# Optimization experiments

Hardware: AMD Instinct MI355X
Metric: run time of the kernel (lower is better)

## Reference

```python
import jax, jax.numpy as jnp
import numpy as np

EPS = 1e-6

def _ln(x):
    m = jnp.mean(x, axis=-1, keepdims=True)
    v = jnp.mean((x - m) ** 2, axis=-1, keepdims=True)
    return (x - m) * jax.lax.rsqrt(v + EPS)

def _quant(x):
    # dynamic per-token symmetric int8 quant (fused_kernels.quant_sum semantics)
    s = jnp.maximum(jnp.max(jnp.abs(x), axis=-1, keepdims=True) / 127.0, 1e-8)
    q = jnp.clip(jnp.round(x / s), -127.0, 127.0)
    return q, s, jnp.sum(q, axis=-1, keepdims=True)

def _w8a8(x, qw, sw, zw, b):
    # W8A8OF16LinearDynamicInputScale: int8 GEMM + zero-point correction via row sum
    q, s, qsum = _quant(x)
    acc = q @ qw.astype(jnp.float32).T - qsum * zw.astype(jnp.float32)
    return acc * (s * sw) + b

def _self_attn(xm, Wqkv, bqkv, Wo, bo, H):
    Bt, S, C = xm.shape
    hd = C // H
    qkv = (xm @ Wqkv.T + bqkv).reshape(Bt, S, 3, H, hd)
    q, k, v = qkv[:, :, 0], qkv[:, :, 1], qkv[:, :, 2]
    attn = jnp.einsum('bqhd,bkhd->bhqk', q * (hd ** -0.5), k).astype(jnp.float32)
    attn = jax.nn.softmax(attn, axis=-1)
    out = jnp.einsum('bhqk,bkhd->bqhd', attn, v).reshape(Bt, S, C)
    return out @ Wo.T + bo

def _cross_attn(x, y, qw_q, sw_q, zw_q, b_q, Wkv, bkv, qw_cp, sw_cp, zw_cp, b_cp, H):
    B, N, C = x.shape
    hd = C // H
    q = _w8a8(x, qw_q, sw_q, zw_q, b_q).reshape(B * N, H, hd)
    kv = (y.reshape(-1, C) @ Wkv.T + bkv).reshape(-1, 2, H, hd)
    k, v = kv[:, 0], kv[:, 1]
    # mask=None path: q (1,B*N,H,hd) attends over all B*M keys (flattened)
    attn = jnp.einsum('qhd,khd->hqk', q * (hd ** -0.5), k).astype(jnp.float32)
    attn = jax.nn.softmax(attn, axis=-1)
    out = jnp.einsum('hqk,khd->qhd', attn, v).reshape(B, N, C)
    return _w8a8(out, qw_cp, sw_cp, zw_cp, b_cp)

def setup_inputs() -> dict:
    key = jax.random.key(0)
    ks = iter(jax.random.split(key, 32))
    B, T, S, C, H, M = 2, 8, 256, 1152, 16, 224
    Dh = int(C * 4.0)
    r = lambda shape, sc=1.0: jax.random.normal(next(ks), shape, dtype=jnp.float32) * sc
    qi = lambda shape: jax.random.randint(next(ks), shape, -127, 128, dtype=jnp.int8)
    zi = lambda shape: jax.random.randint(next(ks), shape, -8, 9, dtype=jnp.int32)
    su = lambda shape: jax.random.uniform(next(ks), shape, minval=0.005, maxval=0.02, dtype=jnp.float32)
    return dict(
        x=r((B, T * S, C)), y=r((B, M, C)), t=r((B, 6 * C)),
        sst=r((6, C), C ** -0.5),
        Wqkv=r((3 * C, C), 0.02), bqkv=r((3 * C,), 0.02),
        Wo=r((C, C), 0.02), bo=r((C,), 0.02),
        Wkv=r((2 * C, C), 0.02), bkv=r((2 * C,), 0.02),
        qw_q=qi((C, C)), sw_q=su((C,)), zw_q=zi((C,)), b_q=r((C,), 0.02),
        qw_cp=qi((C, C)), sw_cp=su((C,)), zw_cp=zi((C,)), b_cp=r((C,), 0.02),
        qw_f1=qi((Dh, C)), sw_f1=su((Dh,)), zw_f1=zi((Dh,)), b_f1=r((Dh,), 0.02),
        qw_f2=qi((C, Dh)), sw_f2=su((C,)), zw_f2=zi((C,)), b_f2=r((C,), 0.02),
        num_heads=H, T=T, S=S,
    )

def reference(x, y, t, sst, Wqkv, bqkv, Wo, bo, Wkv, bkv,
              qw_q, sw_q, zw_q, b_q, qw_cp, sw_cp, zw_cp, b_cp,
              qw_f1, sw_f1, zw_f1, b_f1, qw_f2, sw_f2, zw_f2, b_f2,
              num_heads, T, S):
    B, N, C = x.shape
    mod = sst[None] + t.reshape(B, 6, C)  # (B,6,C)
    shift_msa, scale_msa, gate_msa, shift_mlp, scale_mlp, gate_mlp = (
        mod[:, 0:1], mod[:, 1:2], mod[:, 2:3], mod[:, 3:4], mod[:, 4:5], mod[:, 5:6])
    # --- self-attention (spatial, temporal=False): B (T S) C -> (B T) S C ---
    x_m = _ln(x) * (1.0 + scale_msa) + shift_msa
    x_m = x_m.reshape(B * T, S, C)
    x_m = _self_attn(x_m, Wqkv, bqkv, Wo, bo, num_heads).reshape(B, N, C)
    x = x + gate_msa * x_m  # fused_kernels.gate_residual
    # --- int8 cross-attention ---
    x = x + _cross_attn(x, y, qw_q, sw_q, zw_q, b_q, Wkv, bkv, qw_cp, sw_cp, zw_cp, b_cp, num_heads)
    # --- int8 MLP with fused gelu_quant_sum (tanh-approx GELU) ---
    x_m = _ln(x) * (1.0 + scale_mlp) + shift_mlp
    h = _w8a8(x_m, qw_f1, sw_f1, zw_f1, b_f1)
    h = jax.nn.gelu(h, approximate=True)
    h = _w8a8(h, qw_f2, sw_f2, zw_f2, b_f2)
    x = x + gate_mlp * h
    return x
```

## Files before the change

### kernel.cpp

```cpp
#include <hip/hip_runtime.h>
#include <stdint.h>

typedef unsigned short u16;
typedef _Float16 f16;
typedef f16    f16v8  __attribute__((ext_vector_type(8)));
typedef u16    u16v8  __attribute__((ext_vector_type(8)));
typedef float  f32x4  __attribute__((ext_vector_type(4)));
typedef int    i32x4  __attribute__((ext_vector_type(4)));
typedef int    i32x16 __attribute__((ext_vector_type(16)));

#define MFMA_F16(a,b,c)   __builtin_amdgcn_mfma_f32_16x16x32_f16((a),(b),(c),0,0,0)
#define MFMA_I8_32(a,b,c) __builtin_amdgcn_mfma_i32_32x32x32_i8((a),(b),(c),0,0,0)

__device__ __forceinline__ float b2f(u16 u){ union{unsigned u;float f;}v; v.u=((unsigned)u)<<16; return v.f; }
__device__ __forceinline__ u16 f2b(float f){ union{float f;unsigned u;}v; v.f=f;
  return (u16)((v.u + 0x7fffu + ((v.u>>16)&1u))>>16); }
__device__ __forceinline__ u16 f2h(float f){ f16 h = (f16)f; return __builtin_bit_cast(u16, h); }
__device__ __forceinline__ float h2f(u16 u){ return (float)__builtin_bit_cast(f16, u); }
__device__ __forceinline__ f16v8 ldh8(const u16* p){ return __builtin_bit_cast(f16v8, *(const u16v8*)p); }
__device__ __forceinline__ void gl2lds16(const void* g, void* l){
  __builtin_amdgcn_global_load_lds(
    (const __attribute__((address_space(1))) unsigned int*)g,
    (__attribute__((address_space(3))) unsigned int*)l,
    16, 0, 0);
}
__device__ __forceinline__ float gelu_t(float x){
  float u2 = -1.5957691216057308f*(x + 0.044715f*x*x*x);
  return x * __builtin_amdgcn_rcpf(1.f + __expf(u2));
}

__global__ void mod_add_k(const float* __restrict__ sst, const float* __restrict__ t, float* __restrict__ mod){
  int i = blockIdx.x*256 + threadIdx.x;
  if (i < 2*6*1152) mod[i] = sst[i % 6912] + t[i];
}
__global__ void split2h_k(const float* __restrict__ src, u16* __restrict__ hi, u16* __restrict__ lo, int n){
  int i = blockIdx.x*256 + threadIdx.x;
  if (i >= n) return;
  float v = src[i];
  f16 h = (f16)v;
  hi[i] = __builtin_bit_cast(u16, h);
  lo[i] = f2h(v - (float)h);
}
__global__ void cross_prep_k(const int* __restrict__ qw_q, int8_t* __restrict__ w8q,
                             const int* __restrict__ qw_cp, int8_t* __restrict__ w8cp,
                             const float* __restrict__ Wkv, u16* __restrict__ wkvh, u16* __restrict__ wkvl,
                             const float* __restrict__ y, u16* __restrict__ yf){
  const int S1 = 1327104, S2 = 2654208, S3 = 5308416, S4 = 5824512;
  int i = blockIdx.x*256 + threadIdx.x;
  if (i < S1){ w8q[i] = (int8_t)qw_q[i]; }
  else if (i < S2){ int j = i - S1; w8cp[j] = (int8_t)qw_cp[j]; }
  else if (i < S3){ int j = i - S2; float v = Wkv[j]; f16 h = (f16)v;
    wkvh[j] = __builtin_bit_cast(u16, h); wkvl[j] = f2h(v - (float)h); }
  else if (i < S4){ int j = i - S3; yf[j] = f2h(y[j]); }
}
__global__ void mlp_prep_k(const int* __restrict__ qw_f1, int8_t* __restrict__ w8f1,
                           const int* __restrict__ qw_f2, int8_t* __restrict__ w8f2){
  const int S1 = 5308416, S2 = 10616832;
  int i = blockIdx.x*256 + threadIdx.x;
  if (i < S1){ w8f1[i] = (int8_t)qw_f1[i]; }
  else if (i < S2){ int j = i - S1; w8f2[j] = (int8_t)qw_f2[j]; }
}
__global__ void ln_mod_f16_k(const float* __restrict__ src, u16* __restrict__ xf,
                             const float* __restrict__ mod, int shift_row, int scale_row){
  const int row = blockIdx.x, tid = threadIdx.x;
  const int b = row >> 11;
  const float* ms = mod + ((size_t)b*6 + shift_row)*1152;
  const float* mc = mod + ((size_t)b*6 + scale_row)*1152;
  __shared__ float r1[256], r2[256];
  float s = 0.f, sq = 0.f, vals[5]; int cnt = 0;
  for (int c = tid; c < 1152; c += 256){
    float v = src[(size_t)row*1152+c];
    vals[cnt++] = v; s += v; sq += v*v;
  }
  r1[tid]=s; r2[tid]=sq; __syncthreads();
  for (int st=128; st>0; st>>=1){ if (tid<st){ r1[tid]+=r1[tid+st]; r2[tid]+=r2[tid+st]; } __syncthreads(); }
  float mean = r1[0]*(1.f/1152.f);
  float var  = r2[0]*(1.f/1152.f) - mean*mean;
  float rstd = rsqrtf(var + 1e-6f);
  cnt = 0;
  for (int c = tid; c < 1152; c += 256){
    float v = (vals[cnt++]-mean)*rstd*(1.f+mc[c]) + ms[c];
    xf[(size_t)row*1152+c] = f2h(v);
  }
}
__global__ void rgq_k(const float* __restrict__ x, const float* __restrict__ ao,
                      const float* __restrict__ mod, int gate_row, float* __restrict__ xw,
                      int8_t* __restrict__ q8, float* __restrict__ s_out, int* __restrict__ q_out){
  const int row = blockIdx.x, tid = threadIdx.x;
  const int b = row >> 11;
  const float* mg = mod + ((size_t)b*6 + gate_row)*1152;
  __shared__ float r1[256];
  __shared__ int ri[256];
  float mx = 0.f, vals[5]; int cnt = 0;
  for (int c = tid; c < 1152; c += 256){
    float v = x[(size_t)row*1152+c] + mg[c]*ao[(size_t)row*1152+c];
    xw[(size_t)row*1152+c] = v;
    vals[cnt++] = v; mx = fmaxf(mx, fabsf(v));
  }
  r1[tid]=mx; __syncthreads();
  for (int st=128; st>0; st>>=1){ if (tid<st) r1[tid]=fmaxf(r1[tid],r1[tid+st]); __syncthreads(); }
  const float s_ = fmaxf(r1[0]*(1.f/127.f), 1e-8f);
  const float inv = 1.f/s_;
  int acc = 0; cnt = 0;
  for (int c = tid; c < 1152; c += 256){
    float q = rintf(vals[cnt++]*inv);
    q = fminf(fmaxf(q, -127.f), 127.f);
    q8[(size_t)row*1152+c] = (int8_t)q;
    acc += (int)q;
  }
  ri[tid]=acc; __syncthreads();
  for (int st=128; st>0; st>>=1){ if (tid<st) ri[tid]+=ri[tid+st]; __syncthreads(); }
  if (tid==0){ s_out[row]=s_; q_out[row]=ri[0]; }
}
__global__ void rlq_k(float* __restrict__ xw, const float* __restrict__ add,
                      const float* __restrict__ mod, int shift_row, int scale_row,
                      int8_t* __restrict__ q8, float* __restrict__ s_out, int* __restrict__ q_out){
  const int row = blockIdx.x, tid = threadIdx.x;
  const int b = row >> 11;
  const float* ms = mod + ((size_t)b*6 + shift_row)*1152;
  const float* mc = mod + ((size_t)b*6 + scale_row)*1152;
  __shared__ float r1[256], r2[256];
  __shared__ int ri[256];
  float s = 0.f, sq = 0.f, vals[5]; int cnt = 0;
  for (int c = tid; c < 1152; c += 256){
    float v = xw[(size_t)row*1152+c] + add[(size_t)row*1152+c];
    xw[(size_t)row*1152+c] = v;
    vals[cnt++] = v; s += v; sq += v*v;
  }
  r1[tid]=s; r2[tid]=sq; __syncthreads();
  for (int st=128; st>0; st>>=1){ if (tid<st){ r1[tid]+=r1[tid+st]; r2[tid]+=r2[tid+st]; } __syncthreads(); }
  float mean = r1[0]*(1.f/1152.f);
  float var  = r2[0]*(1.f/1152.f) - mean*mean;
  float rstd = rsqrtf(var + 1e-6f);
  __syncthreads();
  float mx = 0.f; cnt = 0;
  for (int c = tid; c < 1152; c += 256){
    float v = (vals[cnt]-mean)*rstd*(1.f+mc[c]) + ms[c];
    vals[cnt++] = v; mx = fmaxf(mx, fabsf(v));
  }
  r1[tid]=mx; __syncthreads();
  for (int st=128; st>0; st>>=1){ if (tid<st) r1[tid]=fmaxf(r1[tid],r1[tid+st]); __syncthreads(); }
  const float s_ = fmaxf(r1[0]*(1.f/127.f), 1e-8f);
  const float inv = 1.f/s_;
  int acc = 0; cnt = 0;
  for (int c = tid; c < 1152; c += 256){
    float q = rintf(vals[cnt++]*inv);
    q = fminf(fmaxf(q, -127.f), 127.f);
    q8[(size_t)row*1152+c] = (int8_t)q;
    acc += (int)q;
  }
  ri[tid]=acc; __syncthreads();
  for (int st=128; st>0; st>>=1){ if (tid<st) ri[tid]+=ri[tid+st]; __syncthreads(); }
  if (tid==0){ s_out[row]=s_; q_out[row]=ri[0]; }
}
template<int SRC_F32>
__global__ void quant_rows_k(const void* __restrict__ src, int C_,
                             int8_t* __restrict__ q8, float* __restrict__ s_out, int* __restrict__ q_out){
  const int row = blockIdx.x, tid = threadIdx.x;
  __shared__ float red[256];
  __shared__ int redi[256];
  float vals[18];
  float mx = 0.f; int cnt = 0;
  for (int c = tid; c < C_; c += 256){
    float v = SRC_F32 ? ((const float*)src)[(size_t)row*C_+c] : b2f(((const u16*)src)[(size_t)row*C_+c]);
    vals[cnt++] = v;
    mx = fmaxf(mx, fabsf(v));
  }
  red[tid]=mx; __syncthreads();
  for (int st=128; st>0; st>>=1){ if (tid<st) red[tid]=fmaxf(red[tid],red[tid+st]); __syncthreads(); }
  const float s_ = fmaxf(red[0]*(1.f/127.f), 1e-8f);
  const float inv = 1.f/s_;
  int acc = 0; cnt = 0;
  for (int c = tid; c < C_; c += 256){
    float q = rintf(vals[cnt++]*inv);
    q = fminf(fmaxf(q, -127.f), 127.f);
    q8[(size_t)row*C_+c] = (int8_t)q;
    acc += (int)q;
  }
  redi[tid]=acc; __syncthreads();
  for (int st=128; st>0; st>>=1){ if (tid<st) redi[tid]+=redi[tid+st]; __syncthreads(); }
  if (tid==0){ s_out[row]=s_; q_out[row]=redi[0]; }
}

template<int MODE>
__global__ __launch_bounds__(256,4) void gemm_f16k(
    const u16* __restrict__ Af, int lda,
    const u16* __restrict__ Wh, const u16* __restrict__ Wl, int ldw,
    const float* __restrict__ bias, float* __restrict__ out, int ldo, int M, int K,
    u16* __restrict__ e1, u16* __restrict__ e2){
  __shared__ u16 sA[128*32];
  __shared__ u16 sWh[128*32];
  __shared__ u16 sWl[128*32];
  const int tid = threadIdx.x, lane = tid & 63;
  const int wv = tid >> 6, wx = wv & 1, wy = wv >> 1;
  const int quad = lane >> 4, l16 = lane & 15;
  const int m0 = blockIdx.y*128, n0 = blockIdx.x*128;
  f32x4 acc[4][4];
  #pragma unroll
  for (int i=0;i<4;i++)
    #pragma unroll
    for (int j=0;j<4;j++) acc[i][j] = (f32x4){0.f,0.f,0.f,0.f};
  for (int k0=0; k0<K; k0+=32){
    #pragma unroll
    for (int r=0;r<2;r++){
      int slotbase = r*256 + wv*64;
      int slot = slotbase + lane;
      int row = slot >> 2;
      int col8 = ((slot ^ (row>>1)) & 3) * 8;
      int gm = m0 + row; if (gm > M-1) gm = M-1;
      size_t aoff = (size_t)gm*lda + k0 + col8;
      size_t woff = (size_t)(n0+row)*ldw + k0 + col8;
      gl2lds16(Af + aoff, &sA[(size_t)slotbase*8]);
      gl2lds16(Wh + woff, &sWh[(size_t)slotbase*8]);
      gl2lds16(Wl + woff, &sWl[(size_t)slotbase*8]);
    }
    __syncthreads();
    const int cs = ((quad ^ ((l16>>1)&3)) * 8);
    f16v8 a[4], bh[4], bl[4];
    #pragma unroll
    for (int i=0;i<4;i++) a[i] = ldh8(&sA[(wy*64+i*16+l16)*32 + cs]);
    #pragma unroll
    for (int j=0;j<4;j++){
      bh[j] = ldh8(&sWh[(wx*64+j*16+l16)*32 + cs]);
      bl[j] = ldh8(&sWl[(wx*64+j*16+l16)*32 + cs]);
    }
    #pragma unroll
    for (int i=0;i<4;i++)
      #pragma unroll
      for (int j=0;j<4;j++){
        acc[i][j] = MFMA_F16(a[i], bh[j], acc[i][j]);
        acc[i][j] = MFMA_F16(a[i], bl[j], acc[i][j]);
      }
    __syncthreads();
  }
  #pragma unroll
  for (int j=0;j<4;j++){
    int col = n0 + wx*64 + j*16 + l16;
    float bc = bias ? bias[col] : 0.f;
    #pragma unroll
    for (int i=0;i<4;i++)
      #pragma unroll
      for (int r=0;r<4;r++){
        int row = m0 + wy*64 + i*16 + quad*4 + r;
        if (row >= M) continue;
        float v = acc[i][j][r] + bc;
        if (MODE == 0){
          out[(size_t)row*ldo + col] = v;
        } else if (MODE == 1){
          if (col < 2304){
            e1[(size_t)row*2304 + col] = f2h(v);
          } else {
            int vc = col - 2304;
            int hd_ = vc/72, d = vc - hd_*72;
            int z = row >> 8, s2 = row & 255;
            e2[((size_t)(z*16+hd_)*80 + d)*256 + s2] = f2h(v);
          }
        } else {
          if (col < 1152){
            e1[(size_t)row*1152 + col] = f2h(v);
          } else {
            int vc = col - 1152;
            int hd_ = vc/72, d = vc - hd_*72;
            e2[((size_t)hd_*80 + d)*448 + row] = f2h(v);
          }
        }
      }
  }
}

#define QKV_NT 36
__global__ __launch_bounds__(512,2) void gemm_qkv_8ph(
    const u16* __restrict__ Af,
    const u16* __restrict__ Wh_, const u16* __restrict__ Wl_,
    const float* __restrict__ bias,
    u16* __restrict__ qkf, u16* __restrict__ vtf){
  extern __shared__ u16 sm[];
  char* smb = (char*)sm;
  const int tid = threadIdx.x, lane = tid & 63, wv = tid >> 6;
  const int wr = wv >> 2, wc = wv & 3;
  const int quad = lane >> 4, l16 = lane & 15;
  const int c = blockIdx.x & 7, bi = blockIdx.x >> 3;
  const int m0 = (((c>>1)<<2) + (bi&3)) << 8;
  const int n0 = ((c&1)*7 + (bi>>2)) << 8;

  const u16* gA[2]; const u16* gH[2]; const u16* gL[2];
  int sbase[2];
  #pragma unroll
  for (int r=0;r<2;r++){
    int slot = r*512 + tid;
    int row = slot >> 2;
    int col8 = ((slot ^ (row>>1)) & 3) * 8;
    sbase[r] = (r*512 + wv*64) * 16;
    gA[r] = Af + (size_t)(m0+row)*1152 + col8;
    int gn = n0 + row; if (gn > 3455) gn = 3455;
    gH[r] = Wh_ + (size_t)gn*1152 + col8;
    gL[r] = Wl_ + (size_t)gn*1152 + col8;
  }

  #define STG_A(t2,b) { size_t ko=(size_t)(t2)*32; \
    gl2lds16(gA[0]+ko, smb + (b)*49152 + sbase[0]); \
    gl2lds16(gA[1]+ko, smb + (b)*49152 + sbase[1]); }
  #define STG_H(t2,b) { size_t ko=(size_t)(t2)*32; \
    gl2lds16(gH[0]+ko, smb + (b)*49152 + 16384 + sbase[0]); \
    gl2lds16(gH[1]+ko, smb + (b)*49152 + 16384 + sbase[1]); }
  #define STG_L(t2,b) { size_t ko=(size_t)(t2)*32; \
    gl2lds16(gL[0]+ko, smb + (b)*49152 + 32768 + sbase[0]); \
    gl2lds16(gL[1]+ko, smb + (b)*49152 + 32768 + sbase[1]); }

  STG_A(0,0); STG_H(0,0); STG_L(0,0);
  STG_A(1,1); STG_H(1,1); STG_L(1,1);

  const int cs = (quad ^ ((l16>>1)&3)) * 8;
  const int arow = wr*128 + l16;
  const int wrow = wc*64 + l16;

  f32x4 acc[8][4];
  #pragma unroll
  for (int i=0;i<8;i++)
    #pragma unroll
    for (int j=0;j<4;j++) acc[i][j] = (f32x4){0.f,0.f,0.f,0.f};

  f16v8 bh[4], bl[4];

  #define PHASE(p, STAGE_STMT) { \
    const u16* bA = sm + cur*24576; \
    f16v8 a0 = ldh8(bA + (arow + (2*(p))*16)*32 + cs); \
    f16v8 a1 = ldh8(bA + (arow + (2*(p)+1)*16)*32 + cs); \
    if ((p)==0){ \
      const u16* bH = bA + 8192; \
      const u16* bL = bA + 16384; \
      _Pragma("unroll") \
      for (int j=0;j<4;j++){ \
        bh[j] = ldh8(bH + (wrow + j*16)*32 + cs); \
        bl[j] = ldh8(bL + (wrow + j*16)*32 + cs); \
      } \
    } \
    STAGE_STMT; \
    __builtin_amdgcn_s_barrier(); \
    asm volatile("s_waitcnt lgkmcnt(0)" ::: "memory"); \
    __builtin_amdgcn_sched_barrier(0); \
    __builtin_amdgcn_s_setprio(1); \
    _Pragma("unroll") \
    for (int j=0;j<4;j++){ \
      acc[2*(p)][j]   = MFMA_F16(a0, bh[j], acc[2*(p)][j]); \
      acc[2*(p)][j]   = MFMA_F16(a0, bl[j], acc[2*(p)][j]); \
      acc[2*(p)+1][j] = MFMA_F16(a1, bh[j], acc[2*(p)+1][j]); \
      acc[2*(p)+1][j] = MFMA_F16(a1, bl[j], acc[2*(p)+1][j]); \
    } \
    __builtin_amdgcn_s_setprio(0); \
    __builtin_amdgcn_s_barrier(); \
  }

  int cur = 0;
  for (int t = 0; t < QKV_NT-1; ++t){
    const int nxt = (cur == 0) ? 2 : cur - 1;
    asm volatile("s_waitcnt vmcnt(6)" ::: "memory");
    __builtin_amdgcn_s_barrier();
    __builtin_amdgcn_sched_barrier(0);
    const bool pf = (t < QKV_NT-2);
    PHASE(0, if (pf) STG_A(t+2,nxt));
    PHASE(1, if (pf) STG_H(t+2,nxt));
    PHASE(2, if (pf) STG_L(t+2,nxt));
    PHASE(3, );
    cur = (cur == 2) ? 0 : cur + 1;
  }
  asm volatile("s_waitcnt vmcnt(0)" ::: "memory");
  __builtin_amdgcn_s_barrier();
  __builtin_amdgcn_sched_barrier(0);
  PHASE(0, );
  PHASE(1, );
  PHASE(2, );
  PHASE(3, );

  #pragma unroll
  for (int j=0;j<4;j++){
    const int col = n0 + wc*64 + j*16 + l16;
    if (col < 3456){
      const float bc = bias[col];
      if (col < 2304){
        #pragma unroll
        for (int i=0;i<8;i++){
          const size_t rb = (size_t)(m0 + wr*128 + i*16 + quad*4)*2304 + col;
          #pragma unroll
          for (int r=0;r<4;r++)
            qkf[rb + (size_t)r*2304] = f2h(acc[i][j][r] + bc);
        }
      } else {
        const int vc = col - 2304;
        const int hd_ = vc/72, d = vc - hd_*72;
        #pragma unroll
        for (int i=0;i<8;i++){
          #pragma unroll
          for (int r=0;r<4;r++){
            const int row = m0 + wr*128 + i*16 + quad*4 + r;
            const int z = row >> 8, s2 = row & 255;
            vtf[((size_t)(z*16+hd_)*80 + d)*256 + s2] = f2h(acc[i][j][r] + bc);
          }
        }
      }
    }
  }
  #undef PHASE
  #undef STG_A
  #undef STG_H
  #undef STG_L
}

__global__ __launch_bounds__(256,4) void gemm_i8(
    const int8_t* __restrict__ A, int lda, const int8_t* __restrict__ W, int ldw,
    const float* __restrict__ rs, const int* __restrict__ rq,
    const float* __restrict__ sw, const int* __restrict__ zw, const float* __restrict__ bias,
    void* __restrict__ out, int ldo, int M, int K, int do_gelu, int out_f32,
    const float* __restrict__ xwf, const float* __restrict__ modf, int do_final){
  __shared__ int8_t As[128*128];
  __shared__ int8_t Bs[128*128];
  const int tid = threadIdx.x, lane = tid & 63, wv = tid >> 6;
  const int wx = wv & 1, wy = wv >> 1;
  const int l32 = lane & 31, g = lane >> 5;
  int n_idx = blockIdx.x, m_idx = blockIdx.y;
  {
    int nwg = gridDim.x*gridDim.y;
    if ((nwg & 7) == 0){
      int l = blockIdx.y*gridDim.x + blockIdx.x;
      int qq = nwg >> 3;
      int gidx = (l & 7)*qq + (l >> 3);
      n_idx = gidx / (int)gridDim.y;
      m_idx = gidx - n_idx*(int)gridDim.y;
    }
  }
  const int m0 = m_idx*128, n0 = n_idx*128;
  const int srow = lane >> 3, schunk = lane & 7;
  const int scol = ((schunk ^ srow) & 7) * 16;
  i32x16 acc[2][2];
  #pragma unroll
  for (int i=0;i<2;i++)
    #pragma unroll
    for (int j=0;j<2;j++)
      #pragma unroll
      for (int r=0;r<16;r++) acc[i][j][r] = 0;
  for (int k0 = 0; k0 < K; k0 += 128){
    #pragma unroll
    for (int i=0;i<4;i++){
      int rr = (i*4 + wv)*8;
      int gm = m0 + rr + srow; if (gm > M-1) gm = M-1;
      gl2lds16(A + (size_t)gm*lda + k0 + scol, &As[rr*128]);
      int gn = n0 + rr + srow;
      gl2lds16(W + (size_t)gn*ldw + k0 + scol, &Bs[rr*128]);
    }
    __syncthreads();
    #pragma unroll
    for (int kq=0; kq<4; kq++){
      i32x4 af[2], bw[2];
      #pragma unroll
      for (int i=0;i<2;i++){
        int row = wy*64 + i*32 + l32;
        int cs = (((kq*2 + g) ^ (row & 7))) * 16;
        af[i] = *(const i32x4*)&As[row*128 + cs];
      }
      #pragma unroll
      for (int j=0;j<2;j++){
        int row = wx*64 + j*32 + l32;
        int cs = (((kq*2 + g) ^ (row & 7))) * 16;
        bw[j] = *(const i32x4*)&Bs[row*128 + cs];
      }
      #pragma unroll
      for (int i=0;i<2;i++)
        #pragma unroll
        for (int j=0;j<2;j++)
          acc[i][j] = MFMA_I8_32(af[i], bw[j], acc[i][j]);
    }
    __syncthreads();
  }
  #pragma unroll
  for (int j=0;j<2;j++){
    int col = n0 + wx*64 + j*32 + l32;
    float swc = sw[col]; float zwc = (float)zw[col]; float bc = bias[col];
    #pragma unroll
    for (int i=0;i<2;i++)
      #pragma unroll
      for (int r=0;r<16;r++){
        int row = m0 + wy*64 + i*32 + (r&3) + 8*(r>>2) + 4*g;
        if (row < M){
          float v = ((float)acc[i][j][r] - (float)rq[row]*zwc) * (rs[row]*swc) + bc;
          if (do_gelu) v = gelu_t(v);
          if (do_final){
            int bb = row >> 11;
            float ov = xwf[(size_t)row*1152 + col] + modf[((size_t)bb*6+5)*1152 + col]*v;
            ((float*)out)[(size_t)row*ldo + col] = ov;
          } else if (out_f32) ((float*)out)[(size_t)row*ldo + col] = v;
          else                ((u16*)out)[(size_t)row*ldo + col] = f2b(v);
        }
      }
  }
}

__global__ __launch_bounds__(256) void attn_self_f16(
    const u16* __restrict__ qkf, const u16* __restrict__ vtf,
    u16* __restrict__ of, float scale){
  constexpr int NT = 16, PSTR = 264, VSTR = 256;
  __shared__ u16 P[4*16*PSTR];
  const int tid = threadIdx.x, lane = tid & 63, wv = tid >> 6;
  const int quad = lane >> 4, l16 = lane & 15;
  const int h = blockIdx.y, z = blockIdx.z;
  const int qbase = z*256 + blockIdx.x*64;
  const u16* Vth = vtf + (size_t)(z*16+h)*80*VSTR;
  const f16v8 zf = __builtin_bit_cast(f16v8, (u16v8)0);
  const int mrow = qbase + wv*16 + l16;

  f16v8 qf[3];
  #pragma unroll
  for (int t=0;t<3;t++){
    if (t==2 && quad!=0){ qf[t]=zf; }
    else qf[t] = ldh8(qkf + (size_t)mrow*2304 + h*72 + t*32 + (t==2?0:quad*8));
  }
  f32x4 sc[NT];
  #pragma unroll
  for (int nt=0; nt<NT; nt++){
    f32x4 a = {0.f,0.f,0.f,0.f};
    #pragma unroll
    for (int t=0;t<3;t++){
      f16v8 kf = zf;
      if (!(t==2 && quad!=0))
        kf = ldh8(qkf + (size_t)(z*256 + nt*16 + l16)*2304 + 1152 + h*72 + t*32 + (t==2?0:quad*8));
      a = MFMA_F16(qf[t], kf, a);
    }
    sc[nt] = a;
  }
  float mx[4] = {-1e30f,-1e30f,-1e30f,-1e30f};
  #pragma unroll
  for (int nt=0; nt<NT; nt++)
    #pragma unroll
    for (int r=0;r<4;r++){ float v = sc[nt][r]*scale; sc[nt][r]=v; mx[r]=fmaxf(mx[r],v); }
  #pragma unroll
  for (int r=0;r<4;r++)
    for (int d=1; d<16; d<<=1) mx[r] = fmaxf(mx[r], __shfl_xor(mx[r], d, 64));
  float sm[4] = {0.f,0.f,0.f,0.f};
  #pragma unroll
  for (int nt=0; nt<NT; nt++)
    #pragma unroll
    for (int r=0;r<4;r++){ float p = __expf(sc[nt][r]-mx[r]); sc[nt][r]=p; sm[r]+=p; }
  #pragma unroll
  for (int r=0;r<4;r++){
    for (int d=1; d<16; d<<=1) sm[r] += __shfl_xor(sm[r], d, 64);
    sm[r] = 1.f/sm[r];
  }
  u16* Pw = P + wv*16*PSTR;
  #pragma unroll
  for (int nt=0; nt<NT; nt++)
    #pragma unroll
    for (int r=0;r<4;r++)
      Pw[(quad*4+r)*PSTR + nt*16 + l16] = f2h(sc[nt][r]*sm[r]);
  const u16* Pr = P + wv*16*PSTR + (size_t)l16*PSTR;
  #pragma unroll
  for (int dt=0; dt<5; dt++){
    f32x4 o = {0.f,0.f,0.f,0.f};
    #pragma unroll
    for (int kk=0; kk<8; kk++){
      f16v8 pv = ldh8(Pr + kk*32 + quad*8);
      f16v8 bv = ldh8(Vth + (size_t)(dt*16+l16)*VSTR + kk*32 + quad*8);
      o = MFMA_F16(pv, bv, o);
    }
    int d = dt*16 + l16;
    if (d < 72){
      #pragma unroll
      for (int r=0;r<4;r++){
        int row = qbase + wv*16 + quad*4 + r;
        of[(size_t)row*1152 + h*72 + d] = f2h(o[r]);
      }
    }
  }
}

__global__ __launch_bounds__(256) void attn_cross_f16(
    const float* __restrict__ Q32,
    const u16* __restrict__ Kf,
    const u16* __restrict__ Vt,
    float* __restrict__ O, float scale){
  constexpr int NT = 28, PSTR = 456, VSTR = 448;
  __shared__ u16 P[4*16*PSTR];
  const int tid = threadIdx.x, lane = tid & 63, wv = tid >> 6;
  const int quad = lane >> 4, l16 = lane & 15;
  const int h = blockIdx.y;
  const int qbase = blockIdx.x*64;
  const u16* Vth = Vt + (size_t)h*80*VSTR;
  const f16v8 zf = __builtin_bit_cast(f16v8, (u16v8)0);

  const int mrow = qbase + wv*16 + l16;
  const float* qp = Q32 + (size_t)mrow*1152 + h*72;
  f16v8 qf[3];
  #pragma unroll
  for (int t=0;t<3;t++){
    if (t==2 && quad!=0){ qf[t]=zf; continue; }
    u16v8 hv;
    #pragma unroll
    for (int j=0;j<8;j++) hv[j] = f2h(qp[t*32 + (t==2?0:quad*8) + j]);
    qf[t] = __builtin_bit_cast(f16v8, hv);
  }
  f32x4 sc[NT];
  #pragma unroll
  for (int nt=0; nt<NT; nt++){
    f32x4 a = {0.f,0.f,0.f,0.f};
    #pragma unroll
    for (int t=0;t<3;t++){
      f16v8 kf = zf;
      if (!(t==2 && quad!=0))
        kf = ldh8(Kf + (size_t)(nt*16 + l16)*1152 + h*72 + t*32 + (t==2?0:quad*8));
      a = MFMA_F16(qf[t], kf, a);
    }
    sc[nt] = a;
  }
  float mx[4] = {-1e30f,-1e30f,-1e30f,-1e30f};
  #pragma unroll
  for (int nt=0; nt<NT; nt++)
    #pragma unroll
    for (int r=0;r<4;r++){ float v = sc[nt][r]*scale; sc[nt][r]=v; mx[r]=fmaxf(mx[r],v); }
  #pragma unroll
  for (int r=0;r<4;r++)
    for (int d=1; d<16; d<<=1) mx[r] = fmaxf(mx[r], __shfl_xor(mx[r], d, 64));
  float sm[4] = {0.f,0.f,0.f,0.f};
  #pragma unroll
  for (int nt=0; nt<NT; nt++)
    #pragma unroll
    for (int r=0;r<4;r++){ float p = __expf(sc[nt][r]-mx[r]); sc[nt][r]=p; sm[r]+=p; }
  #pragma unroll
  for (int r=0;r<4;r++){
    for (int d=1; d<16; d<<=1) sm[r] += __shfl_xor(sm[r], d, 64);
    sm[r] = 1.f/sm[r];
  }
  u16* Pw = P + wv*16*PSTR;
  #pragma unroll
  for (int nt=0; nt<NT; nt++)
    #pragma unroll
    for (int r=0;r<4;r++)
      Pw[(quad*4+r)*PSTR + nt*16 + l16] = f2h(sc[nt][r]*sm[r]);
  const u16* Pr = P + wv*16*PSTR + (size_t)l16*PSTR;
  #pragma unroll
  for (int dt=0; dt<5; dt++){
    f32x4 o = {0.f,0.f,0.f,0.f};
    #pragma unroll
    for (int kk=0; kk<14; kk++){
      f16v8 pv = ldh8(Pr + kk*32 + quad*8);
      f16v8 bv = ldh8(Vth + (size_t)(dt*16+l16)*VSTR + kk*32 + quad*8);
      o = MFMA_F16(pv, bv, o);
    }
    int d = dt*16 + l16;
    if (d < 72){
      #pragma unroll
      for (int r=0;r<4;r++){
        int row = qbase + wv*16 + quad*4 + r;
        O[(size_t)row*1152 + h*72 + d] = o[r];
      }
    }
  }
}

extern "C" void kernel_launch(void* const* d_in, const int* in_sizes, int n_in,
                              void* d_out, int out_size, void* d_ws, size_t ws_size,
                              hipStream_t stream){
  const float* x    = (const float*)d_in[0];
  const float* y    = (const float*)d_in[1];
  const float* t    = (const float*)d_in[2];
  const float* sst  = (const float*)d_in[3];
  const float* Wqkv = (const float*)d_in[4];
  const float* bqkv = (const float*)d_in[5];
  const float* Wo   = (const float*)d_in[6];
  const float* bo   = (const float*)d_in[7];
  const float* Wkv  = (const float*)d_in[8];
  const float* bkv  = (const float*)d_in[9];
  const int*   qw_q  = (const int*)d_in[10];
  const float* sw_q  = (const float*)d_in[11];
  const int*   zw_q  = (const int*)d_in[12];
  const float* b_q   = (const float*)d_in[13];
  const int*   qw_cp = (const int*)d_in[14];
  const float* sw_cp = (const float*)d_in[15];
  const int*   zw_cp = (const int*)d_in[16];
  const float* b_cp  = (const float*)d_in[17];
  const int*   qw_f1 = (const int*)d_in[18];
  const float* sw_f1 = (const float*)d_in[19];
  const int*   zw_f1 = (const int*)d_in[20];
  const float* b_f1  = (const float*)d_in[21];
  const int*   qw_f2 = (const int*)d_in[22];
  const float* sw_f2 = (const float*)d_in[23];
  const int*   zw_f2 = (const int*)d_in[24];
  const float* b_f2  = (const float*)d_in[25];
  (void)in_sizes; (void)n_in; (void)out_size;

  constexpr size_t SZR = (size_t)4096*1152*4;
  constexpr size_t R0 = 0;
  constexpr size_t R1 = R0 + SZR;
  constexpr size_t R2 = R1 + SZR;
  constexpr size_t R3 = R2 + SZR;
  constexpr size_t R4 = R3 + SZR;
  constexpr size_t R5 = R4 + (size_t)9437184;
  constexpr size_t R6 = R5 + (size_t)9437184;
  constexpr size_t RS = R6 + (size_t)10485760;
  constexpr size_t RQ = RS + (size_t)4096*4;
  constexpr size_t RM = RQ + (size_t)4096*4;
  constexpr size_t WS_NEED = RM + (size_t)2*6*1152*4;
  if (ws_size < WS_NEED) return;

  char* ws = (char*)d_ws;
  float*  xw    = (float*)(ws + R0);
  u16*    wqkvh = (u16*)(ws + R1);
  u16*    wqkvl = (u16*)(ws + R1 + (size_t)3456*1152*2);
  u16*    wkvh  = (u16*)(ws + R1);
  u16*    wkvl  = (u16*)(ws + R1 + (size_t)2304*1152*2);
  u16*    yf    = (u16*)(ws + R1 + (size_t)2*2304*1152*2);
  float*  q32   = (float*)(ws + R1);
  float*  cpout = (float*)(ws + R1);
  int8_t* q8h   = (int8_t*)(ws + R1);
  u16*    qkf   = (u16*)(ws + R2);
  float*  aof   = (float*)(ws + R2);
  u16*    hbuf  = (u16*)(ws + R2);
  u16*    xmf   = (u16*)(ws + R4);
  u16*    of    = (u16*)(ws + R4);
  u16*    kf    = (u16*)(ws + R4 + (size_t)4128768);
  u16*    vtc   = (u16*)(ws + R4 + (size_t)6193152);
  int8_t* w8f2  = (int8_t*)(ws + R4);
  int8_t* w8q   = (int8_t*)(ws + R5);
  int8_t* w8cp  = (int8_t*)(ws + R5 + (size_t)1327104);
  int8_t* w8f1  = (int8_t*)(ws + R5 + (size_t)2654208);
  u16*    vtf   = (u16*)(ws + R6);
  u16*    woh   = (u16*)(ws + R6);
  u16*    wol   = (u16*)(ws + R6 + (size_t)1152*1152*2);
  int8_t* q8x   = (int8_t*)(ws + R6);
  float*  rs    = (float*)(ws + RS);
  int*    rq    = (int*)(ws + RQ);
  float*  mod   = (float*)(ws + RM);

  const float scale = 0.11785113019775793f;

  static bool attr_set = false;
  if (!attr_set){
    hipFuncSetAttribute(reinterpret_cast<const void*>(gemm_qkv_8ph),
                        hipFuncAttributeMaxDynamicSharedMemorySize, 3*49152);
    attr_set = true;
  }

  mod_add_k<<<(2*6*1152+255)/256,256,0,stream>>>(sst, t, mod);

  ln_mod_f16_k<<<4096,256,0,stream>>>(x, xmf, mod, 0, 1);
  split2h_k<<<(3456*1152+255)/256,256,0,stream>>>(Wqkv, wqkvh, wqkvl, 3456*1152);
  gemm_qkv_8ph<<<dim3(224),dim3(512),3*49152,stream>>>(xmf, wqkvh, wqkvl, bqkv, qkf, vtf);
  attn_self_f16<<<dim3(4,16,16),256,0,stream>>>(qkf, vtf, of, scale);
  split2h_k<<<(1152*1152+255)/256,256,0,stream>>>(Wo, woh, wol, 1152*1152);
  gemm_f16k<0><<<dim3(9,32),256,0,stream>>>(of,1152, woh,wol,1152, bo, aof,1152, 4096,1152, nullptr,nullptr);
  rgq_k<<<4096,256,0,stream>>>(x, aof, mod, 2, xw, q8x, rs, rq);

  cross_prep_k<<<(5824512+255)/256,256,0,stream>>>(qw_q,w8q, qw_cp,w8cp, Wkv,wkvh,wkvl, y,yf);
  gemm_f16k<2><<<dim3(18,4),256,0,stream>>>(yf,1152, wkvh,wkvl,1152, bkv, nullptr,0, 448,1152, kf,vtc);
  gemm_i8<<<dim3(9,32),256,0,stream>>>(q8x,1152, w8q,1152, rs,rq, sw_q,zw_q,b_q, q32,1152, 4096,1152, 0, 1, nullptr,nullptr,0);
  attn_cross_f16<<<dim3(64,16),256,0,stream>>>(q32, kf, vtc, aof, scale);
  quant_rows_k<1><<<4096,256,0,stream>>>(aof, 1152, q8x, rs, rq);
  gemm_i8<<<dim3(9,32),256,0,stream>>>(q8x,1152, w8cp,1152, rs,rq, sw_cp,zw_cp,b_cp, cpout,1152, 4096,1152, 0, 1, nullptr,nullptr,0);

  rlq_k<<<4096,256,0,stream>>>(xw, cpout, mod, 3, 4, q8x, rs, rq);
  mlp_prep_k<<<(10616832+255)/256,256,0,stream>>>(qw_f1, w8f1, qw_f2, w8f2);
  gemm_i8<<<dim3(36,32),256,0,stream>>>(q8x,1152, w8f1,1152, rs,rq, sw_f1,zw_f1,b_f1, hbuf,4608, 4096,1152, 1, 0, nullptr,nullptr,0);
  quant_rows_k<0><<<4096,256,0,stream>>>(hbuf, 4608, q8h, rs, rq);
  gemm_i8<<<dim3(9,32),256,0,stream>>>(q8h,4608, w8f2,4608, rs,rq, sw_f2,zw_f2,b_f2, d_out,1152, 4096,4608, 0, 1, xw,mod,1);
}
```

Baseline: 769.4 us.

## Add triple-buffered int8 GEMM with async LDS loads for N=1152 GEMMs

Adds a new int8 MFMA GEMM that stages 128-wide K tiles into a three-deep LDS ring using direct global-to-LDS loads with XOR swizzle. It waits on vmcnt so the load for tile t+2 overlaps compute on tile t. It also remaps workgroup ids for locality and raises wave priority around MFMA bursts. It replaces the cross-attention q/proj GEMMs and the MLP fc2 GEMM to hide global memory latency, at the cost of 96KB of dynamic LDS per block, which limits occupancy to one block per CU.

```diff
diff --git a/kernel.cpp b/kernel.cpp
--- a/kernel.cpp
+++ b/kernel.cpp
@@ -492,6 +492,131 @@
         }
       }
   }
+}
+
+__global__ __launch_bounds__(256,1) void gemm_i8_pipe(
+    const int8_t* __restrict__ A, int lda, const int8_t* __restrict__ W, int ldw,
+    const float* __restrict__ rs, const int* __restrict__ rq,
+    const float* __restrict__ sw, const int* __restrict__ zw, const float* __restrict__ bias,
+    void* __restrict__ out, int ldo, int M, int K, int do_gelu, int out_f32,
+    const float* __restrict__ xwf, const float* __restrict__ modf, int do_final){
+  extern __shared__ char smb[];
+  const int tid = threadIdx.x, lane = tid & 63, wv = tid >> 6;
+  const int wx = wv & 1, wy = wv >> 1;
+  const int l32 = lane & 31, g = lane >> 5;
+  int n_idx = blockIdx.x, m_idx = blockIdx.y;
+  {
+    int nwg = gridDim.x*gridDim.y;
+    if ((nwg & 7) == 0){
+      int l = blockIdx.y*gridDim.x + blockIdx.x;
+      int qq = nwg >> 3;
+      int gidx = (l & 7)*qq + (l >> 3);
+      n_idx = gidx / (int)gridDim.y;
+      m_idx = gidx - n_idx*(int)gridDim.y;
+    }
+  }
+  const int m0 = m_idx*128, n0 = n_idx*128;
+  const int srow = lane >> 3, schunk = lane & 7;
+  const int scol = ((schunk ^ srow) & 7) * 16;
+
+  const int8_t* gA[4]; const int8_t* gB[4]; int lb_[4];
+  #pragma unroll
+  for (int i=0;i<4;i++){
+    int rr = (i*4 + wv)*8;
+    int gm = m0 + rr + srow; if (gm > M-1) gm = M-1;
+    int gn = n0 + rr + srow;
+    gA[i] = A + (size_t)gm*lda + scol;
+    gB[i] = W + (size_t)gn*ldw + scol;
+    lb_[i] = rr*128;
+  }
+  #define STAGE_P(t2,b) { size_t ko=(size_t)(t2)*128; \
+    _Pragma("unroll") \
+    for (int i=0;i<4;i++){ \
+      gl2lds16(gA[i]+ko, smb + (b)*32768 + lb_[i]); \
+      gl2lds16(gB[i]+ko, smb + (b)*32768 + 16384 + lb_[i]); } }
+
+  i32x16 acc[2][2];
+  #pragma unroll
+  for (int i=0;i<2;i++)
+    #pragma unroll
+    for (int j=0;j<2;j++)
+      #pragma unroll
+      for (int r=0;r<16;r++) acc[i][j][r] = 0;
+
+  const int NK = K >> 7;
+  STAGE_P(0, 0);
+  STAGE_P(1, 1);
+  int cur = 0;
+  for (int t = 0; t < NK; ++t){
+    if (t+1 < NK){
+      asm volatile("s_waitcnt vmcnt(8)" ::: "memory");
+    } else {
+      asm volatile("s_waitcnt vmcnt(0)" ::: "memory");
+    }
+    __builtin_amdgcn_s_barrier();
+    __builtin_amdgcn_sched_barrier(0);
+    if (t+2 < NK){
+      int nxt = cur + 2; if (nxt >= 3) nxt -= 3;
+      STAGE_P(t+2, nxt);
+    }
+    const char* bufA = smb + cur*32768;
+    const char* bufB = bufA + 16384;
+    #pragma unroll
+    for (int ph=0; ph<2; ph++){
+      i32x4 af[2][2], bw[2][2];
+      #pragma unroll
+      for (int hh=0; hh<2; hh++){
+        const int kq = ph*2 + hh;
+        #pragma unroll
+        for (int i=0;i<2;i++){
+          int row = wy*64 + i*32 + l32;
+          int cs2 = (((kq*2 + g) ^ (row & 7))) * 16;
+          af[hh][i] = *(const i32x4*)(bufA + row*128 + cs2);
+        }
+        #pragma unroll
+        for (int j=0;j<2;j++){
+          int row = wx*64 + j*32 + l32;
+          int cs2 = (((kq*2 + g) ^ (row & 7))) * 16;
+          bw[hh][j] = *(const i32x4*)(bufB + row*128 + cs2);
+        }
+      }
+      asm volatile("s_waitcnt lgkmcnt(0)" ::: "memory");
+      __builtin_amdgcn_sched_barrier(0);
+      __builtin_amdgcn_s_setprio(1);
+      #pragma unroll
+      for (int hh=0; hh<2; hh++)
+        #pragma unroll
+        for (int i=0;i<2;i++)
+          #pragma unroll
+          for (int j=0;j<2;j++)
+            acc[i][j] = MFMA_I8_32(af[hh][i], bw[hh][j], acc[i][j]);
+      __builtin_amdgcn_s_setprio(0);
+    }
+    cur = (cur == 2) ? 0 : cur + 1;
+  }
+
+  #pragma unroll
+  for (int j=0;j<2;j++){
+    int col = n0 + wx*64 + j*32 + l32;
+    float swc = sw[col]; float zwc = (float)zw[col]; float bc = bias[col];
+    #pragma unroll
+    for (int i=0;i<2;i++)
+      #pragma unroll
+      for (int r=0;r<16;r++){
+        int row = m0 + wy*64 + i*32 + (r&3) + 8*(r>>2) + 4*g;
+        if (row < M){
+          float v = ((float)acc[i][j][r] - (float)rq[row]*zwc) * (rs[row]*swc) + bc;
+          if (do_gelu) v = gelu_t(v);
+          if (do_final){
+            int bb = row >> 11;
+            float ov = xwf[(size_t)row*1152 + col] + modf[((size_t)bb*6+5)*1152 + col]*v;
+            ((float*)out)[(size_t)row*ldo + col] = ov;
+          } else if (out_f32) ((float*)out)[(size_t)row*ldo + col] = v;
+          else                ((u16*)out)[(size_t)row*ldo + col] = f2b(v);
+        }
+      }
+  }
+  #undef STAGE_P
 }
 
 __global__ __launch_bounds__(256) void attn_self_f16(
@@ -734,6 +859,8 @@
   if (!attr_set){
     hipFuncSetAttribute(reinterpret_cast<const void*>(gemm_qkv_8ph),
                         hipFuncAttributeMaxDynamicSharedMemorySize, 3*49152);
+    hipFuncSetAttribute(reinterpret_cast<const void*>(gemm_i8_pipe),
+                        hipFuncAttributeMaxDynamicSharedMemorySize, 3*32768);
     attr_set = true;
   }
 
@@ -749,14 +876,14 @@
 
   cross_prep_k<<<(5824512+255)/256,256,0,stream>>>(qw_q,w8q, qw_cp,w8cp, Wkv,wkvh,wkvl, y,yf);
   gemm_f16k<2><<<dim3(18,4),256,0,stream>>>(yf,1152, wkvh,wkvl,1152, bkv, nullptr,0, 448,1152, kf,vtc);
-  gemm_i8<<<dim3(9,32),256,0,stream>>>(q8x,1152, w8q,1152, rs,rq, sw_q,zw_q,b_q, q32,1152, 4096,1152, 0, 1, nullptr,nullptr,0);
+  gemm_i8_pipe<<<dim3(9,32),256,3*32768,stream>>>(q8x,1152, w8q,1152, rs,rq, sw_q,zw_q,b_q, q32,1152, 4096,1152, 0, 1, nullptr,nullptr,0);
   attn_cross_f16<<<dim3(64,16),256,0,stream>>>(q32, kf, vtc, aof, scale);
   quant_rows_k<1><<<4096,256,0,stream>>>(aof, 1152, q8x, rs, rq);
-  gemm_i8<<<dim3(9,32),256,0,stream>>>(q8x,1152, w8cp,1152, rs,rq, sw_cp,zw_cp,b_cp, cpout,1152, 4096,1152, 0, 1, nullptr,nullptr,0);
+  gemm_i8_pipe<<<dim3(9,32),256,3*32768,stream>>>(q8x,1152, w8cp,1152, rs,rq, sw_cp,zw_cp,b_cp, cpout,1152, 4096,1152, 0, 1, nullptr,nullptr,0);
 
   rlq_k<<<4096,256,0,stream>>>(xw, cpout, mod, 3, 4, q8x, rs, rq);
   mlp_prep_k<<<(10616832+255)/256,256,0,stream>>>(qw_f1, w8f1, qw_f2, w8f2);
   gemm_i8<<<dim3(36,32),256,0,stream>>>(q8x,1152, w8f1,1152, rs,rq, sw_f1,zw_f1,b_f1, hbuf,4608, 4096,1152, 1, 0, nullptr,nullptr,0);
   quant_rows_k<0><<<4096,256,0,stream>>>(hbuf, 4608, q8h, rs, rq);
-  gemm_i8<<<dim3(9,32),256,0,stream>>>(q8h,4608, w8f2,4608, rs,rq, sw_f2,zw_f2,b_f2, d_out,1152, 4096,4608, 0, 1, xw,mod,1);
-}
+  gemm_i8_pipe<<<dim3(9,32),256,3*32768,stream>>>(q8h,4608, w8f2,4608, rs,rq, sw_f2,zw_f2,b_f2, d_out,1152, 4096,4608, 0, 1, xw,mod,1);
+}
```

After: 830.7 us. +8.0%, slower.
